# Performance work log

Measured on AMD Instinct MI355X. Metric: run time of the kernel, lower is better.

## Reference

```python
import jax, jax.numpy as jnp
import numpy as np

SQRT2PI = float(np.sqrt(2.0 * np.pi))
DN = 20          # disperse_number / heat-map side
OUT_CH = 32      # conv out_channels
MINY, MAXY, SD = 0.0, 50.0, 0.3
BN_EPS = 1e-5


def setup_inputs() -> dict:
    key = jax.random.key(0)
    ks = jax.random.split(key, 8)
    N_ATOM, N_ELE, N_NODE = 65536, 16384, 8192
    oe = jax.random.uniform(ks[0], (N_ATOM, 17), dtype=jnp.float32)
    node_ele_idx = jax.random.randint(ks[1], (N_ELE, 4), 0, N_ATOM, dtype=jnp.int64)
    ele_atom_idx = jax.random.randint(ks[2], (N_NODE, 2), 0, N_ELE, dtype=jnp.int64)
    conv_w = jax.random.normal(ks[3], (OUT_CH, 1, 3, 3), dtype=jnp.float32) * 0.1
    conv_b = jnp.zeros((OUT_CH,), jnp.float32)
    bn_gamma = jnp.ones((OUT_CH,), jnp.float32)
    bn_beta = jnp.zeros((OUT_CH,), jnp.float32)
    w1 = jax.random.normal(ks[4], (500, OUT_CH * DN * DN), dtype=jnp.float32) * 0.01
    b1 = jnp.zeros((500,), jnp.float32)
    w2 = jax.random.normal(ks[5], (60, 500), dtype=jnp.float32) * 0.05
    b2 = jnp.zeros((60,), jnp.float32)
    return dict(oe=oe, node_ele_idx=node_ele_idx, ele_atom_idx=ele_atom_idx,
                conv_w=conv_w, conv_b=conv_b, bn_gamma=bn_gamma, bn_beta=bn_beta,
                w1=w1, b1=b1, w2=w2, b2=b2)


def _distribute(rows):
    # rows: (N_node, 17). Gaussian soft histogram onto DN-point grid per row,
    # per-value max-normalization, masked sum over the 17 values, row max-normalization.
    grid = jnp.linspace(MINY, MAXY, DN).astype(rows.dtype)          # (DN,)
    mask = (rows > 0.0) & (rows < 110.0)                            # filter 0 < y < 110
    pdf = jnp.exp(-(grid[None, None, :] - rows[:, :, None]) ** 2 /
                  (2.0 * SD * SD)) / (SQRT2PI * SD)                 # (N, 17, DN)
    m = jnp.max(pdf, axis=-1, keepdims=True)
    pdf = jnp.where(m != 0, pdf / m, pdf)                           # yi / max(yi)
    pdf = pdf * mask[:, :, None]
    s = jnp.sum(pdf, axis=1)                                        # (N, DN)
    smax = jnp.max(s, axis=-1, keepdims=True)
    return jnp.where(smax != 0, s / smax, s)


def reference(oe, node_ele_idx, ele_atom_idx, conv_w, conv_b,
              bn_gamma, bn_beta, w1, b1, w2, b2):
    # merge_idx(oe, node_ele_idx): gather atoms per element, mean-reduce
    g = jnp.mean(oe[node_ele_idx], axis=1)                          # (N_ele, 17)
    g = g / jnp.linalg.norm(g, axis=1, keepdims=True)
    # merge_idx(..., ele_atom_idx, method='sum')
    h = jnp.sum(g[ele_atom_idx], axis=1)                            # (N_node, 17)
    d = _distribute(h)                                              # (N_node, DN)
    # outer-sum heat map: a[n,i,j] = d[n,j], b[n,i,j] = d[n,i]
    x1 = (d[:, None, :] + d[:, :, None])[:, None, :, :]             # (N_node,1,DN,DN)
    x = jax.lax.conv_general_dilated(
        x1, conv_w, window_strides=(1, 1), padding='SAME',
        dimension_numbers=('NCHW', 'OIHW', 'NCHW')) + conv_b[None, :, None, None]
    # Dropout2d is identity in eval mode. BatchNorm2d: training-mode batch stats.
    mu = jnp.mean(x, axis=(0, 2, 3), keepdims=True)
    var = jnp.var(x, axis=(0, 2, 3), keepdims=True)
    xn = (x - mu) / jnp.sqrt(var + BN_EPS)
    x = xn * bn_gamma[None, :, None, None] + bn_beta[None, :, None, None] + x1
    x = x.reshape(x.shape[0], -1)                                   # (N_node, 32*400)
    x = jax.nn.relu(x @ w1.T + b1)
    x = x @ w2.T + b2
    return x.reshape(x.shape[0], 20, 3)
```

## Files before the change

kernel.cpp:

```cpp
#include <hip/hip_runtime.h>
#include <hip/hip_bf16.h>
#include <math.h>

#define NFEAT 17
#define DN 20
#define OCH 32
#define H1 500
#define H2 60

#define DK 4

#define OFF_D      0
#define OFF_MOMP   32768
#define OFF_ACOEF  36352
#define OFF_COEFC  36384
#define OFF_WQ     36416
#define OFF_WP     36704
#define OFF_U4     36992
#define OFF_CST    38992
#define OFF_W2T    39504

#define NBW 256

#define TB1 128
__global__ __launch_bounds__(TB1) void k_gd(const float* __restrict__ oe,
                                            const int* __restrict__ nei,
                                            const int* __restrict__ eai,
                                            const float* __restrict__ w2,
                                            const float* __restrict__ convw,
                                            float* __restrict__ dmat,
                                            float* __restrict__ momp,
                                            float* __restrict__ w2t,
                                            float* __restrict__ wq,
                                            float* __restrict__ wp, int n_node) {
  int nbd = (n_node + 63) / 64;
  int tid = threadIdx.x;
  if ((int)blockIdx.x >= nbd) {
    int tb = blockIdx.x - nbd;
    if (tb < 8) {
      __shared__ float sT[64][61];
      int o0 = tb * 64;
      int lo = tid & 63, j2 = tid >> 6;
      for (int j = j2; j < H2; j += 2)
        if (o0 + lo < H1) sT[lo][j] = w2[(size_t)j * H1 + o0 + lo];
      __syncthreads();
      int jj = tid & 63, o2 = tid >> 6;
      for (int ol = o2; ol < 64; ol += 2) {
        int o = o0 + ol;
        if (o < H1) w2t[(size_t)o * 64 + jj] = (jj < H2) ? sT[ol][jj] : 0.f;
      }
    } else if (tid < OCH) {
      int c = tid;
      float w[3][3];
#pragma unroll
      for (int p = 0; p < 3; ++p)
#pragma unroll
        for (int q = 0; q < 3; ++q) w[p][q] = convw[c * 9 + p * 3 + q];
#pragma unroll
      for (int p = 0; p < 3; ++p) {
        wq[(c * 3 + p) * 3 + 0] = w[p][1] + w[p][2];
        wq[(c * 3 + p) * 3 + 1] = w[p][0] + w[p][1] + w[p][2];
        wq[(c * 3 + p) * 3 + 2] = w[p][0] + w[p][1];
      }
#pragma unroll
      for (int q = 0; q < 3; ++q) {
        wp[(c * 3 + q) * 3 + 0] = w[1][q] + w[2][q];
        wp[(c * 3 + q) * 3 + 1] = w[0][q] + w[1][q] + w[2][q];
        wp[(c * 3 + q) * 3 + 2] = w[0][q] + w[1][q];
      }
    }
    return;
  }

  __shared__ float dls[64][5];
  int nl = tid >> 1, half = tid & 1;
  int n = blockIdx.x * 64 + nl;

  float v[NFEAT];
#pragma unroll
  for (int f = 0; f < NFEAT; ++f) v[f] = 0.f;
  if (n < n_node) {
    int e = eai[(size_t)n * 2 + half];
    float a4[NFEAT];
#pragma unroll
    for (int f = 0; f < NFEAT; ++f) a4[f] = 0.f;
#pragma unroll
    for (int m = 0; m < 4; ++m) {
      int at = nei[(size_t)e * 4 + m];
      const float* row = oe + (size_t)at * NFEAT;
#pragma unroll
      for (int f = 0; f < NFEAT; ++f) a4[f] += row[f];
    }
    float nrm = 0.f;
#pragma unroll
    for (int f = 0; f < NFEAT; ++f) { float t = a4[f] * 0.25f; a4[f] = t; nrm += t * t; }
    float inv = 1.0f / sqrtf(nrm);
#pragma unroll
    for (int f = 0; f < NFEAT; ++f) v[f] = a4[f] * inv;
  }
  float h[NFEAT];
#pragma unroll
  for (int f = 0; f < NFEAT; ++f) h[f] = v[f] + __shfl_xor(v[f], 1);

  const float step = 50.0f / 19.0f;
  const float inv2 = 1.0f / (2.0f * 0.3f * 0.3f);
  float s0 = 0.f, s1 = 0.f, s2 = 0.f, s3 = 0.f;
  int f0 = half ? 9 : 0, f1 = half ? NFEAT : 9;
  for (int f = f0; f < f1; ++f) {
    float y = h[f];
    if (!(y > 0.0f && y < 110.0f)) continue;
    float t0 = -y, t1 = step - y, t2 = 2.f * step - y, t3 = 3.f * step - y;
    float e0 = __expf(-t0 * t0 * inv2);
    float e1 = __expf(-t1 * t1 * inv2);
    float e2 = __expf(-t2 * t2 * inv2);
    float e3 = __expf(-t3 * t3 * inv2);
    float m = fmaxf(fmaxf(e0, e1), fmaxf(e2, e3));
    if (m > 0.f) {
      float im = 1.0f / m;
      s0 += e0 * im; s1 += e1 * im; s2 += e2 * im; s3 += e3 * im;
    }
  }
  s0 += __shfl_xor(s0, 1); s1 += __shfl_xor(s1, 1);
  s2 += __shfl_xor(s2, 1); s3 += __shfl_xor(s3, 1);
  float smax = fmaxf(fmaxf(s0, s1), fmaxf(s2, s3));
  float ism = (smax > 0.f) ? 1.0f / smax : 1.0f;
  float d0 = s0 * ism, d1 = s1 * ism, d2 = s2 * ism, d3 = s3 * ism;

  if (half == 0) {
    dls[nl][0] = d0; dls[nl][1] = d1; dls[nl][2] = d2; dls[nl][3] = d3;
    if (n < n_node)
      *(float4*)(dmat + (size_t)n * DK) = make_float4(d0, d1, d2, d3);
  }
  __syncthreads();

  if (tid < 14) {
    int u = tid;
    float acc = 0.f;
    if (u < 10) {
      int a = 0, rem = u;
      while (rem >= DK - a) { rem -= DK - a; ++a; }
      int b = a + rem;
      for (int l = 0; l < 64; ++l) acc += dls[l][a] * dls[l][b];
    } else {
      int a = u - 10;
      for (int l = 0; l < 64; ++l) acc += dls[l][a];
    }
    momp[(size_t)u * NBW + blockIdx.x] = acc;
  }
}

__global__ __launch_bounds__(512) void k_coef(const float* __restrict__ momp, int nbd,
                                              const float* __restrict__ convw,
                                              const float* __restrict__ convb,
                                              const float* __restrict__ gamma,
                                              const float* __restrict__ beta,
                                              float* __restrict__ acoef,
                                              float* __restrict__ coefc, int n_node) {
  int c = blockIdx.x;
  int tid = threadIdx.x;
  __shared__ float P[DN * DN];
  __shared__ float S[DN];
  __shared__ float red1[512], red2[512];
  if (tid < DN * DN) P[tid] = 0.f;
  if (tid >= 448 && tid < 448 + DN) S[tid - 448] = 0.f;
  __syncthreads();
  if (tid < 14) {
    float acc = 0.f;
    const float4* row4 = (const float4*)(momp + (size_t)tid * NBW);
    int nb4 = nbd >> 2;
    for (int b = 0; b < nb4; ++b) {
      float4 t = row4[b];
      acc += t.x + t.y + t.z + t.w;
    }
    for (int b = nb4 << 2; b < nbd; ++b) acc += momp[(size_t)tid * NBW + b];
    if (tid < 10) {
      int a = 0, rem = tid;
      while (rem >= DK - a) { rem -= DK - a; ++a; }
      int b = a + rem;
      P[a * DN + b] = acc; P[b * DN + a] = acc;
    } else {
      S[tid - 10] = acc;
    }
  }
  __syncthreads();

  float w[3][3];
#pragma unroll
  for (int p = 0; p < 3; ++p)
#pragma unroll
    for (int q = 0; q < 3; ++q) w[p][q] = convw[c * 9 + p * 3 + q];
  float b_c = convb[c];

  float ssq = 0.f, sm = 0.f;
  if (tid < DN * DN) {
    int i = tid / DN, j = tid % DN;
    bool iv[3] = { i > 0, true, i < DN - 1 };
    bool jv[3] = { j > 0, true, j < DN - 1 };
    int idxs[6]; float cf[6]; int nt = 0;
#pragma unroll
    for (int p = 0; p < 3; ++p) if (iv[p]) {
      float cc = 0.f;
#pragma unroll
      for (int q = 0; q < 3; ++q) if (jv[q]) cc += w[p][q];
      idxs[nt] = i - 1 + p; cf[nt] = cc; ++nt;
    }
#pragma unroll
    for (int q = 0; q < 3; ++q) if (jv[q]) {
      float cc = 0.f;
#pragma unroll
      for (int p = 0; p < 3; ++p) if (iv[p]) cc += w[p][q];
      idxs[nt] = j - 1 + q; cf[nt] = cc; ++nt;
    }
    float q1 = 0.f, q2 = 0.f;
    for (int u = 0; u < nt; ++u) {
      q2 += cf[u] * S[idxs[u]];
      for (int v2 = 0; v2 < nt; ++v2)
        q1 += cf[u] * cf[v2] * P[idxs[u] * DN + idxs[v2]];
    }
    ssq = q1 + 2.f * b_c * q2;
    sm = q2;
  }
  red1[tid] = ssq; red2[tid] = sm;
  __syncthreads();
  for (int st = 256; st > 0; st >>= 1) {
    if (tid < st) { red1[tid] += red1[tid + st]; red2[tid] += red2[tid + st]; }
    __syncthreads();
  }
  if (tid == 0) {
    float Nt = (float)n_node * 400.f;
    float S1 = red2[0] + Nt * b_c;
    float S2 = red1[0] + Nt * b_c * b_c;
    float mu = S1 / Nt;
    float var = S2 / Nt - mu * mu;
    float a = gamma[c] / sqrtf(var + 1e-5f);
    acoef[c] = a;
    coefc[c] = a * (b_c - mu) + beta[c];
  }
}

__global__ __launch_bounds__(512) void k_buildU(const float* __restrict__ w1,
                                                const float* __restrict__ b1,
                                                const float* __restrict__ acoef,
                                                const float* __restrict__ coefc,
                                                const float* __restrict__ wq,
                                                const float* __restrict__ wp,
                                                float* __restrict__ U4,
                                                float* __restrict__ Cst) {
  int o = blockIdx.x;
  int tid = threadIdx.x;
  __shared__ float sW[OCH * DN * 21];
  __shared__ float rowRS[OCH][DN], colCS[OCH][DN];
  __shared__ float rowRW[3][OCH][DN], colCW[3][OCH][DN];
  __shared__ float swq[288], swp[288], sac[OCH], scc[OCH], red[OCH];
  for (int idx = tid; idx < 288; idx += 512) { swq[idx] = wq[idx]; swp[idx] = wp[idx]; }
  if (tid < OCH) { sac[tid] = acoef[tid]; scc[tid] = coefc[tid]; }
  __syncthreads();

  const float* wbase = w1 + (size_t)o * (OCH * DN * DN);

  for (int pair = tid; pair < OCH * DN; pair += 512) {
    int c = pair / DN, i = pair - c * DN;
    const float4* r = (const float4*)(wbase + pair * DN);
    float4 v0 = r[0], v1 = r[1], v2 = r[2], v3 = r[3], v4 = r[4];
    float first = v0.x, last = v4.w;
    float rs = v0.x + v0.y + v0.z + v0.w + v1.x + v1.y + v1.z + v1.w +
               v2.x + v2.y + v2.z + v2.w + v3.x + v3.y + v3.z + v3.w +
               v4.x + v4.y + v4.z + v4.w;
    float mid = rs - first - last;
#pragma unroll
    for (int p = 0; p < 3; ++p)
      rowRW[p][c][i] = first * swq[(c * 3 + p) * 3 + 0] +
                       mid   * swq[(c * 3 + p) * 3 + 1] +
                       last  * swq[(c * 3 + p) * 3 + 2];
    rowRS[c][i] = rs;
    float* dst = &sW[pair * 21];
    dst[0] = v0.x; dst[1] = v0.y; dst[2] = v0.z; dst[3] = v0.w;
    dst[4] = v1.x; dst[5] = v1.y; dst[6] = v1.z; dst[7] = v1.w;
    dst[8] = v2.x; dst[9] = v2.y; dst[10] = v2.z; dst[11] = v2.w;
    dst[12] = v3.x; dst[13] = v3.y; dst[14] = v3.z; dst[15] = v3.w;
    dst[16] = v4.x; dst[17] = v4.y; dst[18] = v4.z; dst[19] = v4.w;
  }
  __syncthreads();

  for (int pair = tid; pair < OCH * DN; pair += 512) {
    int c = pair / DN, j = pair - c * DN;
    const float* src = &sW[c * DN * 21 + j];
    float cs = 0.f, first = 0.f, last = 0.f;
#pragma unroll
    for (int i = 0; i < DN; ++i) {
      float vv = src[i * 21];
      cs += vv;
      if (i == 0) first = vv;
      if (i == DN - 1) last = vv;
    }
    float mid = cs - first - last;
#pragma unroll
    for (int q = 0; q < 3; ++q)
      colCW[q][c][j] = first * swp[(c * 3 + q) * 3 + 0] +
                       mid   * swp[(c * 3 + q) * 3 + 1] +
                       last  * swp[(c * 3 + q) * 3 + 2];
    colCS[c][j] = cs;
  }
  __syncthreads();

  if (tid < DK) {
    int a = tid;
    float u = 0.f;
#pragma unroll
    for (int c = 0; c < OCH; ++c) {
      float plain = rowRS[c][a] + colCS[c][a];
      float m = rowRW[1][c][a] + colCW[1][c][a];
      m += rowRW[0][c][a + 1] + colCW[0][c][a + 1];
      if (a > 0) m += rowRW[2][c][a - 1] + colCW[2][c][a - 1];
      u += plain + sac[c] * m;
    }
    U4[o * DK + a] = u;
  } else if (tid >= 64 && tid < 64 + OCH) {
    int c = tid - 64;
    float s = 0.f;
#pragma unroll
    for (int i = 0; i < DN; ++i) s += rowRS[c][i];
    red[c] = scc[c] * s;
  }
  __syncthreads();
  if (tid == 0) {
    float s = 0.f;
#pragma unroll
    for (int c = 0; c < OCH; ++c) s += red[c];
    Cst[o] = b1[o] + s;
  }
}

#define NTN 16
__global__ __launch_bounds__(256, 4) void k_final(const float* __restrict__ dmat,
                                                  const float* __restrict__ U4,
                                                  const float* __restrict__ Cst,
                                                  const float* __restrict__ w2t,
                                                  const float* __restrict__ b2,
                                                  float* __restrict__ out, int n_node) {
  __shared__ float h1s[H1][20];
  __shared__ float pacc[4][NTN][64];
  int tid = threadIdx.x;
  int n0 = blockIdx.x * NTN;

  {
    int node = tid & 15, kq = tid >> 4;
    float4 d4 = make_float4(0.f, 0.f, 0.f, 0.f);
    if (n0 + node < n_node)
      d4 = *(const float4*)(dmat + (size_t)(n0 + node) * DK);
    for (int k = kq; k < H1; k += 16) {
      float4 u4 = *(const float4*)(U4 + (size_t)k * DK);
      float z = Cst[k] + u4.x * d4.x + u4.y * d4.y + u4.z * d4.z + u4.w * d4.w;
      h1s[k][node] = fmaxf(z, 0.f);
    }
  }
  __syncthreads();

  {
    int w = tid >> 6;
    int lane = tid & 63;
    int q = lane >> 4;
    int og = lane & 15;
    float a0x = 0.f, a0y = 0.f, a0z = 0.f, a0w = 0.f;
    float a1x = 0.f, a1y = 0.f, a1z = 0.f, a1w = 0.f;
    float a2x = 0.f, a2y = 0.f, a2z = 0.f, a2w = 0.f;
    float a3x = 0.f, a3y = 0.f, a3z = 0.f, a3w = 0.f;
    int k0 = w * 125, k1 = k0 + 125;
    for (int k = k0; k < k1; ++k) {
      float4 hv = *(const float4*)&h1s[k][q * 4];
      float4 wv = *(const float4*)(w2t + (size_t)k * 64 + og * 4);
      a0x += hv.x * wv.x; a0y += hv.x * wv.y; a0z += hv.x * wv.z; a0w += hv.x * wv.w;
      a1x += hv.y * wv.x; a1y += hv.y * wv.y; a1z += hv.y * wv.z; a1w += hv.y * wv.w;
      a2x += hv.z * wv.x; a2y += hv.z * wv.y; a2z += hv.z * wv.z; a2w += hv.z * wv.w;
      a3x += hv.w * wv.x; a3y += hv.w * wv.y; a3z += hv.w * wv.z; a3w += hv.w * wv.w;
    }
    *(float4*)&pacc[w][q * 4 + 0][og * 4] = make_float4(a0x, a0y, a0z, a0w);
    *(float4*)&pacc[w][q * 4 + 1][og * 4] = make_float4(a1x, a1y, a1z, a1w);
    *(float4*)&pacc[w][q * 4 + 2][og * 4] = make_float4(a2x, a2y, a2z, a2w);
    *(float4*)&pacc[w][q * 4 + 3][og * 4] = make_float4(a3x, a3y, a3z, a3w);
  }
  __syncthreads();

  for (int idx = tid; idx < NTN * H2; idx += 256) {
    int n = idx / H2, o = idx - n * H2;
    float vv = pacc[0][n][o] + pacc[1][n][o] + pacc[2][n][o] + pacc[3][n][o] + b2[o];
    if (n0 + n < n_node) out[(size_t)(n0 + n) * H2 + o] = vv;
  }
}

extern "C" void kernel_launch(void* const* d_in, const int* in_sizes, int n_in,
                              void* d_out, int out_size, void* d_ws, size_t ws_size,
                              hipStream_t stream) {
  const float* oe    = (const float*)d_in[0];
  const int*   nei   = (const int*)d_in[1];
  const int*   eai   = (const int*)d_in[2];
  const float* convw = (const float*)d_in[3];
  const float* convb = (const float*)d_in[4];
  const float* gamma = (const float*)d_in[5];
  const float* beta  = (const float*)d_in[6];
  const float* w1    = (const float*)d_in[7];
  const float* b1    = (const float*)d_in[8];
  const float* w2    = (const float*)d_in[9];
  const float* b2    = (const float*)d_in[10];
  float* out = (float*)d_out;
  float* ws  = (float*)d_ws;

  int n_node = in_sizes[2] / 2;

  float* dmat  = ws + OFF_D;
  float* momp  = ws + OFF_MOMP;
  float* acoef = ws + OFF_ACOEF;
  float* coefc = ws + OFF_COEFC;
  float* wq    = ws + OFF_WQ;
  float* wp    = ws + OFF_WP;
  float* U4    = ws + OFF_U4;
  float* Cst   = ws + OFF_CST;
  float* w2t   = ws + OFF_W2T;

  int nbd = (n_node + 63) / 64;
  k_gd<<<nbd + 9, TB1, 0, stream>>>(oe, nei, eai, w2, convw,
                                    dmat, momp, w2t, wq, wp, n_node);
  k_coef<<<OCH, 512, 0, stream>>>(momp, nbd, convw, convb, gamma, beta,
                                  acoef, coefc, n_node);
  k_buildU<<<H1, 512, 0, stream>>>(w1, b1, acoef, coefc, wq, wp, U4, Cst);
  k_final<<<(n_node + NTN - 1) / NTN, 256, 0, stream>>>(dmat, U4, Cst, w2t, b2, out, n_node);
}
```

Measured before the change: 55.15 us.

## Fold BatchNorm coefficient kernel into buildU and spread atom gather across threads

Removes the separate k_coef launch. Per-channel conv moment matrices (MT) are now precomputed in the extra k_gd blocks, and each k_buildU block recomputes the BN scale and shift from the reduced block partials. The gather stage now uses 8 threads per node, one per atom, and shuffle reductions, with 32 nodes per block and 256-thread blocks. This cuts a kernel launch and improves memory parallelism in the gather. In exchange, every one of the 500 buildU blocks redundantly reduces momp, and nbd doubles to 256 partials.

```diff
diff --git a/kernel.cpp b/kernel.cpp
--- a/kernel.cpp
+++ b/kernel.cpp
@@ -12,17 +12,17 @@
 
 #define OFF_D      0
 #define OFF_MOMP   32768
-#define OFF_ACOEF  36352
-#define OFF_COEFC  36384
-#define OFF_WQ     36416
-#define OFF_WP     36704
-#define OFF_U4     36992
-#define OFF_CST    38992
-#define OFF_W2T    39504
+#define OFF_WQ     36352
+#define OFF_WP     36640
+#define OFF_MT     36928
+#define OFF_U4     37376
+#define OFF_CST    39376
+#define OFF_W2T    39888
 
 #define NBW 256
 
-#define TB1 128
+#define TB1 256
+#define NPB1 32
 __global__ __launch_bounds__(TB1) void k_gd(const float* __restrict__ oe,
                                             const int* __restrict__ nei,
                                             const int* __restrict__ eai,
@@ -32,81 +32,131 @@
                                             float* __restrict__ momp,
                                             float* __restrict__ w2t,
                                             float* __restrict__ wq,
-                                            float* __restrict__ wp, int n_node) {
-  int nbd = (n_node + 63) / 64;
+                                            float* __restrict__ wp,
+                                            float* __restrict__ MT, int n_node) {
+  int nbd = (n_node + NPB1 - 1) / NPB1;
   int tid = threadIdx.x;
   if ((int)blockIdx.x >= nbd) {
     int tb = blockIdx.x - nbd;
     if (tb < 8) {
       __shared__ float sT[64][61];
       int o0 = tb * 64;
-      int lo = tid & 63, j2 = tid >> 6;
-      for (int j = j2; j < H2; j += 2)
+      int lo = tid & 63, jr = tid >> 6;
+      for (int j = jr; j < H2; j += 4)
         if (o0 + lo < H1) sT[lo][j] = w2[(size_t)j * H1 + o0 + lo];
       __syncthreads();
-      int jj = tid & 63, o2 = tid >> 6;
-      for (int ol = o2; ol < 64; ol += 2) {
+      int jj = tid & 63, orr = tid >> 6;
+      for (int ol = orr; ol < 64; ol += 4) {
         int o = o0 + ol;
         if (o < H1) w2t[(size_t)o * 64 + jj] = (jj < H2) ? sT[ol][jj] : 0.f;
       }
-    } else if (tid < OCH) {
-      int c = tid;
-      float w[3][3];
+    } else {
+      __shared__ float swqL[288], swpL[288];
+      __shared__ float MTs[OCH][14];
+      if (tid < OCH) {
+        int c = tid;
+        float w[3][3];
+#pragma unroll
+        for (int p = 0; p < 3; ++p)
+#pragma unroll
+          for (int q = 0; q < 3; ++q) w[p][q] = convw[c * 9 + p * 3 + q];
+#pragma unroll
+        for (int p = 0; p < 3; ++p) {
+          float v0 = w[p][1] + w[p][2], v1 = w[p][0] + w[p][1] + w[p][2], v2 = w[p][0] + w[p][1];
+          wq[(c * 3 + p) * 3 + 0] = v0; swqL[(c * 3 + p) * 3 + 0] = v0;
+          wq[(c * 3 + p) * 3 + 1] = v1; swqL[(c * 3 + p) * 3 + 1] = v1;
+          wq[(c * 3 + p) * 3 + 2] = v2; swqL[(c * 3 + p) * 3 + 2] = v2;
+        }
+#pragma unroll
+        for (int q = 0; q < 3; ++q) {
+          float v0 = w[1][q] + w[2][q], v1 = w[0][q] + w[1][q] + w[2][q], v2 = w[0][q] + w[1][q];
+          wp[(c * 3 + q) * 3 + 0] = v0; swpL[(c * 3 + q) * 3 + 0] = v0;
+          wp[(c * 3 + q) * 3 + 1] = v1; swpL[(c * 3 + q) * 3 + 1] = v1;
+          wp[(c * 3 + q) * 3 + 2] = v2; swpL[(c * 3 + q) * 3 + 2] = v2;
+        }
+      }
+      for (int idx = tid; idx < OCH * 14; idx += TB1) MTs[idx / 14][idx % 14] = 0.f;
+      __syncthreads();
+      int c = tid & 31, grp = tid >> 5;
+      float wqr[3][3], wpr[3][3];
 #pragma unroll
       for (int p = 0; p < 3; ++p)
 #pragma unroll
-        for (int q = 0; q < 3; ++q) w[p][q] = convw[c * 9 + p * 3 + q];
-#pragma unroll
-      for (int p = 0; p < 3; ++p) {
-        wq[(c * 3 + p) * 3 + 0] = w[p][1] + w[p][2];
-        wq[(c * 3 + p) * 3 + 1] = w[p][0] + w[p][1] + w[p][2];
-        wq[(c * 3 + p) * 3 + 2] = w[p][0] + w[p][1];
+        for (int k = 0; k < 3; ++k) {
+          wqr[p][k] = swqL[(c * 3 + p) * 3 + k];
+          wpr[p][k] = swpL[(c * 3 + p) * 3 + k];
+        }
+      float T0 = 0, T1 = 0, T2 = 0, T3 = 0;
+      float M0 = 0, M1 = 0, M2 = 0, M3 = 0, M4 = 0, M5 = 0, M6 = 0, M7 = 0, M8 = 0, M9 = 0;
+      for (int pos = grp; pos < DN * DN; pos += 8) {
+        int i = pos / DN, j = pos - (pos / DN) * DN;
+        int icls = (i == 0) ? 0 : ((i == DN - 1) ? 2 : 1);
+        int jcls = (j == 0) ? 0 : ((j == DN - 1) ? 2 : 1);
+        float t0 = 0, t1 = 0, t2 = 0, t3 = 0;
+        {
+          int p;
+          p = 0 - i + 1; if ((unsigned)p <= 2u) t0 += wqr[p][jcls];
+          p = 1 - i + 1; if ((unsigned)p <= 2u) t1 += wqr[p][jcls];
+          p = 2 - i + 1; if ((unsigned)p <= 2u) t2 += wqr[p][jcls];
+          p = 3 - i + 1; if ((unsigned)p <= 2u) t3 += wqr[p][jcls];
+          p = 0 - j + 1; if ((unsigned)p <= 2u) t0 += wpr[p][icls];
+          p = 1 - j + 1; if ((unsigned)p <= 2u) t1 += wpr[p][icls];
+          p = 2 - j + 1; if ((unsigned)p <= 2u) t2 += wpr[p][icls];
+          p = 3 - j + 1; if ((unsigned)p <= 2u) t3 += wpr[p][icls];
+        }
+        T0 += t0; T1 += t1; T2 += t2; T3 += t3;
+        M0 += t0 * t0; M1 += t0 * t1; M2 += t0 * t2; M3 += t0 * t3;
+        M4 += t1 * t1; M5 += t1 * t2; M6 += t1 * t3;
+        M7 += t2 * t2; M8 += t2 * t3; M9 += t3 * t3;
       }
-#pragma unroll
-      for (int q = 0; q < 3; ++q) {
-        wp[(c * 3 + q) * 3 + 0] = w[1][q] + w[2][q];
-        wp[(c * 3 + q) * 3 + 1] = w[0][q] + w[1][q] + w[2][q];
-        wp[(c * 3 + q) * 3 + 2] = w[0][q] + w[1][q];
-      }
+      atomicAdd(&MTs[c][0], T0); atomicAdd(&MTs[c][1], T1);
+      atomicAdd(&MTs[c][2], T2); atomicAdd(&MTs[c][3], T3);
+      atomicAdd(&MTs[c][4], M0); atomicAdd(&MTs[c][5], M1);
+      atomicAdd(&MTs[c][6], M2); atomicAdd(&MTs[c][7], M3);
+      atomicAdd(&MTs[c][8], M4); atomicAdd(&MTs[c][9], M5);
+      atomicAdd(&MTs[c][10], M6); atomicAdd(&MTs[c][11], M7);
+      atomicAdd(&MTs[c][12], M8); atomicAdd(&MTs[c][13], M9);
+      __syncthreads();
+      for (int idx = tid; idx < OCH * 14; idx += TB1) MT[idx] = MTs[idx / 14][idx % 14];
     }
     return;
   }
 
-  __shared__ float dls[64][5];
-  int nl = tid >> 1, half = tid & 1;
-  int n = blockIdx.x * 64 + nl;
-
-  float v[NFEAT];
-#pragma unroll
-  for (int f = 0; f < NFEAT; ++f) v[f] = 0.f;
+  __shared__ float dls[NPB1][4];
+  int nl = tid >> 3, t = tid & 7;
+  int half = t >> 2, m = t & 3;
+  int n = blockIdx.x * NPB1 + nl;
+
+  float a[NFEAT];
+#pragma unroll
+  for (int f = 0; f < NFEAT; ++f) a[f] = 0.f;
   if (n < n_node) {
     int e = eai[(size_t)n * 2 + half];
-    float a4[NFEAT];
-#pragma unroll
-    for (int f = 0; f < NFEAT; ++f) a4[f] = 0.f;
-#pragma unroll
-    for (int m = 0; m < 4; ++m) {
-      int at = nei[(size_t)e * 4 + m];
-      const float* row = oe + (size_t)at * NFEAT;
-#pragma unroll
-      for (int f = 0; f < NFEAT; ++f) a4[f] += row[f];
-    }
-    float nrm = 0.f;
-#pragma unroll
-    for (int f = 0; f < NFEAT; ++f) { float t = a4[f] * 0.25f; a4[f] = t; nrm += t * t; }
-    float inv = 1.0f / sqrtf(nrm);
-#pragma unroll
-    for (int f = 0; f < NFEAT; ++f) v[f] = a4[f] * inv;
-  }
+    int at = nei[(size_t)e * 4 + m];
+    const float* row = oe + (size_t)at * NFEAT;
+#pragma unroll
+    for (int f = 0; f < NFEAT; ++f) a[f] = row[f];
+  }
+#pragma unroll
+  for (int f = 0; f < NFEAT; ++f) {
+    a[f] += __shfl_xor(a[f], 1);
+    a[f] += __shfl_xor(a[f], 2);
+  }
+  float nrm = 0.f;
+#pragma unroll
+  for (int f = 0; f < NFEAT; ++f) { float v = a[f] * 0.25f; a[f] = v; nrm += v * v; }
+  float inv = (n < n_node) ? 1.0f / sqrtf(nrm) : 0.f;
   float h[NFEAT];
 #pragma unroll
-  for (int f = 0; f < NFEAT; ++f) h[f] = v[f] + __shfl_xor(v[f], 1);
+  for (int f = 0; f < NFEAT; ++f) {
+    float g = a[f] * inv;
+    h[f] = g + __shfl_xor(g, 4);
+  }
 
   const float step = 50.0f / 19.0f;
   const float inv2 = 1.0f / (2.0f * 0.3f * 0.3f);
   float s0 = 0.f, s1 = 0.f, s2 = 0.f, s3 = 0.f;
-  int f0 = half ? 9 : 0, f1 = half ? NFEAT : 9;
-  for (int f = f0; f < f1; ++f) {
+  for (int f = t; f < NFEAT; f += 8) {
     float y = h[f];
     if (!(y > 0.0f && y < 110.0f)) continue;
     float t0 = -y, t1 = step - y, t2 = 2.f * step - y, t3 = 3.f * step - y;
@@ -114,19 +164,21 @@
     float e1 = __expf(-t1 * t1 * inv2);
     float e2 = __expf(-t2 * t2 * inv2);
     float e3 = __expf(-t3 * t3 * inv2);
-    float m = fmaxf(fmaxf(e0, e1), fmaxf(e2, e3));
-    if (m > 0.f) {
-      float im = 1.0f / m;
+    float mx = fmaxf(fmaxf(e0, e1), fmaxf(e2, e3));
+    if (mx > 0.f) {
+      float im = 1.0f / mx;
       s0 += e0 * im; s1 += e1 * im; s2 += e2 * im; s3 += e3 * im;
     }
   }
-  s0 += __shfl_xor(s0, 1); s1 += __shfl_xor(s1, 1);
-  s2 += __shfl_xor(s2, 1); s3 += __shfl_xor(s3, 1);
+#pragma unroll
+  for (int d = 1; d <= 4; d <<= 1) {
+    s0 += __shfl_xor(s0, d); s1 += __shfl_xor(s1, d);
+    s2 += __shfl_xor(s2, d); s3 += __shfl_xor(s3, d);
+  }
   float smax = fmaxf(fmaxf(s0, s1), fmaxf(s2, s3));
   float ism = (smax > 0.f) ? 1.0f / smax : 1.0f;
-  float d0 = s0 * ism, d1 = s1 * ism, d2 = s2 * ism, d3 = s3 * ism;
-
-  if (half == 0) {
+  if (t == 0) {
+    float d0 = s0 * ism, d1 = s1 * ism, d2 = s2 * ism, d3 = s3 * ism;
     dls[nl][0] = d0; dls[nl][1] = d1; dls[nl][2] = d2; dls[nl][3] = d3;
     if (n < n_node)
       *(float4*)(dmat + (size_t)n * DK) = make_float4(d0, d1, d2, d3);
@@ -137,113 +189,28 @@
     int u = tid;
     float acc = 0.f;
     if (u < 10) {
-      int a = 0, rem = u;
-      while (rem >= DK - a) { rem -= DK - a; ++a; }
-      int b = a + rem;
-      for (int l = 0; l < 64; ++l) acc += dls[l][a] * dls[l][b];
+      int aa = 0, rem = u;
+      while (rem >= DK - aa) { rem -= DK - aa; ++aa; }
+      int bb = aa + rem;
+      for (int l = 0; l < NPB1; ++l) acc += dls[l][aa] * dls[l][bb];
     } else {
-      int a = u - 10;
-      for (int l = 0; l < 64; ++l) acc += dls[l][a];
+      int aa = u - 10;
+      for (int l = 0; l < NPB1; ++l) acc += dls[l][aa];
     }
     momp[(size_t)u * NBW + blockIdx.x] = acc;
-  }
-}
-
-__global__ __launch_bounds__(512) void k_coef(const float* __restrict__ momp, int nbd,
-                                              const float* __restrict__ convw,
-                                              const float* __restrict__ convb,
-                                              const float* __restrict__ gamma,
-                                              const float* __restrict__ beta,
-                                              float* __restrict__ acoef,
-                                              float* __restrict__ coefc, int n_node) {
-  int c = blockIdx.x;
-  int tid = threadIdx.x;
-  __shared__ float P[DN * DN];
-  __shared__ float S[DN];
-  __shared__ float red1[512], red2[512];
-  if (tid < DN * DN) P[tid] = 0.f;
-  if (tid >= 448 && tid < 448 + DN) S[tid - 448] = 0.f;
-  __syncthreads();
-  if (tid < 14) {
-    float acc = 0.f;
-    const float4* row4 = (const float4*)(momp + (size_t)tid * NBW);
-    int nb4 = nbd >> 2;
-    for (int b = 0; b < nb4; ++b) {
-      float4 t = row4[b];
-      acc += t.x + t.y + t.z + t.w;
-    }
-    for (int b = nb4 << 2; b < nbd; ++b) acc += momp[(size_t)tid * NBW + b];
-    if (tid < 10) {
-      int a = 0, rem = tid;
-      while (rem >= DK - a) { rem -= DK - a; ++a; }
-      int b = a + rem;
-      P[a * DN + b] = acc; P[b * DN + a] = acc;
-    } else {
-      S[tid - 10] = acc;
-    }
-  }
-  __syncthreads();
-
-  float w[3][3];
-#pragma unroll
-  for (int p = 0; p < 3; ++p)
-#pragma unroll
-    for (int q = 0; q < 3; ++q) w[p][q] = convw[c * 9 + p * 3 + q];
-  float b_c = convb[c];
-
-  float ssq = 0.f, sm = 0.f;
-  if (tid < DN * DN) {
-    int i = tid / DN, j = tid % DN;
-    bool iv[3] = { i > 0, true, i < DN - 1 };
-    bool jv[3] = { j > 0, true, j < DN - 1 };
-    int idxs[6]; float cf[6]; int nt = 0;
-#pragma unroll
-    for (int p = 0; p < 3; ++p) if (iv[p]) {
-      float cc = 0.f;
-#pragma unroll
-      for (int q = 0; q < 3; ++q) if (jv[q]) cc += w[p][q];
-      idxs[nt] = i - 1 + p; cf[nt] = cc; ++nt;
-    }
-#pragma unroll
-    for (int q = 0; q < 3; ++q) if (jv[q]) {
-      float cc = 0.f;
-#pragma unroll
-      for (int p = 0; p < 3; ++p) if (iv[p]) cc += w[p][q];
-      idxs[nt] = j - 1 + q; cf[nt] = cc; ++nt;
-    }
-    float q1 = 0.f, q2 = 0.f;
-    for (int u = 0; u < nt; ++u) {
-      q2 += cf[u] * S[idxs[u]];
-      for (int v2 = 0; v2 < nt; ++v2)
-        q1 += cf[u] * cf[v2] * P[idxs[u] * DN + idxs[v2]];
-    }
-    ssq = q1 + 2.f * b_c * q2;
-    sm = q2;
-  }
-  red1[tid] = ssq; red2[tid] = sm;
-  __syncthreads();
-  for (int st = 256; st > 0; st >>= 1) {
-    if (tid < st) { red1[tid] += red1[tid + st]; red2[tid] += red2[tid + st]; }
-    __syncthreads();
-  }
-  if (tid == 0) {
-    float Nt = (float)n_node * 400.f;
-    float S1 = red2[0] + Nt * b_c;
-    float S2 = red1[0] + Nt * b_c * b_c;
-    float mu = S1 / Nt;
-    float var = S2 / Nt - mu * mu;
-    float a = gamma[c] / sqrtf(var + 1e-5f);
-    acoef[c] = a;
-    coefc[c] = a * (b_c - mu) + beta[c];
   }
 }
 
 __global__ __launch_bounds__(512) void k_buildU(const float* __restrict__ w1,
                                                 const float* __restrict__ b1,
-                                                const float* __restrict__ acoef,
-                                                const float* __restrict__ coefc,
+                                                const float* __restrict__ convb,
+                                                const float* __restrict__ gamma,
+                                                const float* __restrict__ beta,
                                                 const float* __restrict__ wq,
                                                 const float* __restrict__ wp,
+                                                const float* __restrict__ momp,
+                                                const float* __restrict__ MT,
+                                                int nbd, int n_node,
                                                 float* __restrict__ U4,
                                                 float* __restrict__ Cst) {
   int o = blockIdx.x;
@@ -252,8 +219,46 @@
   __shared__ float rowRS[OCH][DN], colCS[OCH][DN];
   __shared__ float rowRW[3][OCH][DN], colCW[3][OCH][DN];
   __shared__ float swq[288], swp[288], sac[OCH], scc[OCH], red[OCH];
+  __shared__ float mred[14][4], phat[10], S4[4];
   for (int idx = tid; idx < 288; idx += 512) { swq[idx] = wq[idx]; swp[idx] = wp[idx]; }
-  if (tid < OCH) { sac[tid] = acoef[tid]; scc[tid] = coefc[tid]; }
+  if (tid < 56) {
+    int u = tid >> 2, part = tid & 3;
+    int b0 = part * 64, bend = (b0 + 64 < nbd) ? b0 + 64 : nbd;
+    float acc = 0.f;
+    const float* mp = momp + (size_t)u * NBW;
+    for (int b = b0; b < bend; ++b) acc += mp[b];
+    mred[u][part] = acc;
+  }
+  __syncthreads();
+  if (tid < 14) {
+    float v = mred[tid][0] + mred[tid][1] + mred[tid][2] + mred[tid][3];
+    if (tid < 10) {
+      int aa = 0, rem = tid;
+      while (rem >= DK - aa) { rem -= DK - aa; ++aa; }
+      int bb = aa + rem;
+      phat[tid] = (aa == bb ? 1.f : 2.f) * v;
+    } else {
+      S4[tid - 10] = v;
+    }
+  }
+  __syncthreads();
+  if (tid < OCH) {
+    int c = tid;
+    const float* mt = MT + c * 14;
+    float q2 = mt[0] * S4[0] + mt[1] * S4[1] + mt[2] * S4[2] + mt[3] * S4[3];
+    float q1 = 0.f;
+#pragma unroll
+    for (int u = 0; u < 10; ++u) q1 += mt[4 + u] * phat[u];
+    float b_c = convb[c];
+    float Nt = (float)n_node * 400.f;
+    float S1 = q2 + Nt * b_c;
+    float S2 = q1 + 2.f * b_c * q2 + Nt * b_c * b_c;
+    float mu = S1 / Nt;
+    float var = S2 / Nt - mu * mu;
+    float aa = gamma[c] / sqrtf(var + 1e-5f);
+    sac[c] = aa;
+    scc[c] = aa * (b_c - mu) + beta[c];
+  }
   __syncthreads();
 
   const float* wbase = w1 + (size_t)o * (OCH * DN * DN);
@@ -407,21 +412,19 @@
 
   int n_node = in_sizes[2] / 2;
 
-  float* dmat  = ws + OFF_D;
-  float* momp  = ws + OFF_MOMP;
-  float* acoef = ws + OFF_ACOEF;
-  float* coefc = ws + OFF_COEFC;
-  float* wq    = ws + OFF_WQ;
-  float* wp    = ws + OFF_WP;
-  float* U4    = ws + OFF_U4;
-  float* Cst   = ws + OFF_CST;
-  float* w2t   = ws + OFF_W2T;
-
-  int nbd = (n_node + 63) / 64;
+  float* dmat = ws + OFF_D;
+  float* momp = ws + OFF_MOMP;
+  float* wq   = ws + OFF_WQ;
+  float* wp   = ws + OFF_WP;
+  float* MT   = ws + OFF_MT;
+  float* U4   = ws + OFF_U4;
+  float* Cst  = ws + OFF_CST;
+  float* w2t  = ws + OFF_W2T;
+
+  int nbd = (n_node + NPB1 - 1) / NPB1;
   k_gd<<<nbd + 9, TB1, 0, stream>>>(oe, nei, eai, w2, convw,
-                                    dmat, momp, w2t, wq, wp, n_node);
-  k_coef<<<OCH, 512, 0, stream>>>(momp, nbd, convw, convb, gamma, beta,
-                                  acoef, coefc, n_node);
-  k_buildU<<<H1, 512, 0, stream>>>(w1, b1, acoef, coefc, wq, wp, U4, Cst);
+                                    dmat, momp, w2t, wq, wp, MT, n_node);
+  k_buildU<<<H1, 512, 0, stream>>>(w1, b1, convb, gamma, beta, wq, wp,
+                                   momp, MT, nbd, n_node, U4, Cst);
   k_final<<<(n_node + NTN - 1) / NTN, 256, 0, stream>>>(dmat, U4, Cst, w2t, b2, out, n_node);
 }
```

Result: slower. 74.05 us (+34.3%).
